# Performance work log

Measured on AMD Instinct MI355X. Metric: run time of the kernel, lower is better.

## Reference

```python
import jax, jax.numpy as jnp
import numpy as np

HEADS = 8
DIM_HEAD = 40
SCALE = DIM_HEAD ** -0.5


def setup_inputs() -> dict:
    key = jax.random.key(0)
    ks = jax.random.split(key, 6)
    B, S, D = 2, 4096, 320  # batch, seq (64x64 latent), query_dim
    inner = HEADS * DIM_HEAD  # 320
    s = 0.02
    return {
        "x": jax.random.normal(ks[0], (B, S, D), jnp.float32),
        "Wq": jax.random.normal(ks[1], (inner, D), jnp.float32) * s,
        "Wk": jax.random.normal(ks[2], (inner, D), jnp.float32) * s,
        "Wv": jax.random.normal(ks[3], (inner, D), jnp.float32) * s,
        "Wout": jax.random.normal(ks[4], (D, inner), jnp.float32) * s,
        "bout": jnp.zeros((D,), jnp.float32),
    }


def _split_heads(t):
    # [B, S, h*d] -> [B, h, S, d]
    B, S, _ = t.shape
    return t.reshape(B, S, HEADS, DIM_HEAD).transpose(0, 2, 1, 3)


def reference(x, Wq, Wk, Wv, Wout, bout):
    # self-attention path (context=None): k/v come from x
    q = _split_heads(x @ Wq.T)  # [B,h,S,d]
    k = _split_heads(x @ Wk.T)
    v = _split_heads(x @ Wv.T)
    # scores: materialized O(S^2) attention as in the torch einsum
    attn = jax.nn.softmax(jnp.einsum('bhid,bhjd->bhij', q, k) * SCALE, axis=-1)
    out = jnp.einsum('bhij,bhjd->bhid', attn, v)  # [B,h,S,d]
    B, _, S, _ = out.shape
    out = out.transpose(0, 2, 1, 3).reshape(B, S, HEADS * DIM_HEAD)
    return out @ Wout.T + bout  # to_out (dropout=0 -> identity)
```

## Files before the change

### kernel.cpp

```cpp
#include <hip/hip_runtime.h>

#define HEADS 8
#define DHEAD 40
#define SEQ   4096
#define BATCH 2
#define INNER 320
#define NBH   16
#define QSCALE ((float)(0.15811388300841897 * 1.4426950408889634))

typedef _Float16 f16;
typedef __attribute__((ext_vector_type(4)))  _Float16 half4;
typedef __attribute__((ext_vector_type(8)))  _Float16 half8;
typedef __attribute__((ext_vector_type(16))) float    f32x16;

#define XN4   (BATCH * SEQ * INNER / 4)
#define WQKV4 (3 * INNER * INNER / 4)
#define WOUT4 (INNER * INNER / 4)
#define CONV_TOTAL (XN4 + WQKV4 + WOUT4)

__global__ __launch_bounds__(256)
void convert_kernel(const float* __restrict__ x,
                    const float* __restrict__ Wq,
                    const float* __restrict__ Wk,
                    const float* __restrict__ Wv,
                    const float* __restrict__ Wout,
                    f16* __restrict__ xh, f16* __restrict__ wh,
                    f16* __restrict__ wouth)
{
    int i = blockIdx.x * 256 + threadIdx.x;
    if (i >= CONV_TOTAL) return;
    float4 v;
    f16* dst;
    float sc = 1.0f;
    if (i < XN4) {
        v = ((const float4*)x)[i];
        dst = xh + 4 * (size_t)i;
    } else if (i < XN4 + WQKV4) {
        int j = i - XN4;
        if (j < 25600)      { v = ((const float4*)Wq)[j]; sc = QSCALE; }
        else if (j < 51200) { v = ((const float4*)Wk)[j - 25600]; }
        else                { v = ((const float4*)Wv)[j - 51200]; }
        dst = wh + 4 * (size_t)j;
    } else {
        int j = i - XN4 - WQKV4;
        v = ((const float4*)Wout)[j];
        dst = wouth + 4 * (size_t)j;
    }
    half4 hh;
    hh.x = (f16)(v.x * sc); hh.y = (f16)(v.y * sc);
    hh.z = (f16)(v.z * sc); hh.w = (f16)(v.w * sc);
    *(half4*)dst = hh;
}

#define ASTR 72

__global__ __launch_bounds__(256)
void qkv_gemm_kernel(const f16* __restrict__ xh, const f16* __restrict__ wh,
                     f16* __restrict__ q, f16* __restrict__ k,
                     f16* __restrict__ vt)
{
    __shared__ f16 lds[(128 + 64) * ASTR];
    f16* As = lds;
    f16* Bs = lds + 128 * ASTR;

    const int tid  = threadIdx.x;
    const int m0   = blockIdx.y * 128;
    const int by   = blockIdx.x;
    const int wsel = by / 5;
    const int nb0  = (by % 5) * 64;
    const int wave = tid >> 6, lane = tid & 63, m = lane & 31, half = lane >> 5;

    f32x16 acc[2];
    #pragma unroll
    for (int i = 0; i < 16; i++) { acc[0][i] = 0.f; acc[1][i] = 0.f; }

    const f16* wbase = wh + (size_t)by * 64 * 320;

    for (int k0 = 0; k0 < 320; k0 += 64) {
        __syncthreads();
        #pragma unroll
        for (int u = 0; u < 4; u++) {
            int idx = tid + 256 * u;
            int r = idx >> 3, c8 = idx & 7;
            *(uint4*)&As[r * ASTR + c8 * 8] =
                *(const uint4*)&xh[(size_t)(m0 + r) * 320 + k0 + c8 * 8];
        }
        #pragma unroll
        for (int u = 0; u < 2; u++) {
            int idx = tid + 256 * u;
            int r = idx >> 3, c8 = idx & 7;
            *(uint4*)&Bs[r * ASTR + c8 * 8] =
                *(const uint4*)&wbase[(size_t)r * 320 + k0 + c8 * 8];
        }
        __syncthreads();
        #pragma unroll
        for (int c = 0; c < 4; c++) {
            half8 a  = *(const half8*)&As[(wave * 32 + m) * ASTR + c * 16 + half * 8];
            half8 b0 = *(const half8*)&Bs[m * ASTR + c * 16 + half * 8];
            half8 b1 = *(const half8*)&Bs[(32 + m) * ASTR + c * 16 + half * 8];
            acc[0] = __builtin_amdgcn_mfma_f32_32x32x16_f16(a, b0, acc[0], 0, 0, 0);
            acc[1] = __builtin_amdgcn_mfma_f32_32x32x16_f16(a, b1, acc[1], 0, 0, 0);
        }
    }

    if (wsel < 2) {
        f16* dst = (wsel == 0) ? q : k;
        #pragma unroll
        for (int nt = 0; nt < 2; nt++) {
            int nb = nb0 + nt * 32 + m;
            int h  = (nb * 205) >> 13;
            int dd = nb - h * 40;
            #pragma unroll
            for (int reg = 0; reg < 16; reg++) {
                int crow = 4 * half + (reg & 3) + 8 * (reg >> 2);
                int mg = m0 + wave * 32 + crow;
                int b = mg >> 12, s = mg & 4095;
                dst[((size_t)(b * 8 + h) * SEQ + s) * DHEAD + dd] = (f16)acc[nt][reg];
            }
        }
    } else {
        __syncthreads();
        f16* Ct = lds;
        #pragma unroll
        for (int nt = 0; nt < 2; nt++) {
            #pragma unroll
            for (int g = 0; g < 4; g++) {
                half4 hh;
                hh.x = (f16)acc[nt][4 * g + 0]; hh.y = (f16)acc[nt][4 * g + 1];
                hh.z = (f16)acc[nt][4 * g + 2]; hh.w = (f16)acc[nt][4 * g + 3];
                *(half4*)&Ct[(nt * 32 + m) * 136 + wave * 32 + 8 * g + 4 * half] = hh;
            }
        }
        __syncthreads();
        const int b = m0 >> 12, s0 = m0 & 4095;
        #pragma unroll
        for (int u = 0; u < 8; u++) {
            int idx = tid + 256 * u;
            int rl = idx >> 5, c4 = idx & 31;
            int nb = nb0 + rl;
            int h  = (nb * 205) >> 13;
            int dd = nb - h * 40;
            int w4 = c4 & 3;
            int c4p = (c4 & ~3) | ((w4 == 1) ? 2 : (w4 == 2) ? 1 : w4);
            *(uint2*)&vt[((size_t)(b * 8 + h) * DHEAD + dd) * SEQ + s0 + c4p * 4] =
                *(const uint2*)&Ct[rl * 136 + c4 * 4];
        }
    }
}

#define KSTR 56
#define VSTR 72
#define LDS_K 0
#define LDS_V 3584

__global__ __launch_bounds__(256, 4)
void attn_kernel(const f16* __restrict__ q, const f16* __restrict__ k,
                 const f16* __restrict__ vt, f16* __restrict__ y)
{
    __shared__ __align__(16) unsigned char ldsbuf[16896];
    f16*   ldsh = (f16*)ldsbuf;
    float* ldsf = (float*)ldsbuf;

    const int tid = threadIdx.x;
    const int blk = blockIdx.x;
    const int bh = blk >> 6, qt = blk & 63;
    const int b = bh >> 3, h = bh & 7;
    const int q0 = qt * 64;
    const int wave = tid >> 6, lane = tid & 63, m = lane & 31, half = lane >> 5;
    const int qs = wave >> 1, kh = wave & 1;

    if (tid < 128) {
        int key = tid >> 1, off = (tid & 1) * 4;
        *(uint2*)&ldsh[LDS_K + key * KSTR + 40 + off] = make_uint2(0u, 0u);
    }
    for (int i = tid; i < 24 * 16; i += 256) {
        int r = i >> 4, c = (i & 15) * 4;
        uint2 val = (r == 0) ? make_uint2(0x3C003C00u, 0x3C003C00u)
                             : make_uint2(0u, 0u);
        *(uint2*)&ldsh[LDS_V + (40 + r) * VSTR + c] = val;
    }

    half8 zero8;
    #pragma unroll
    for (int j = 0; j < 8; j++) zero8[j] = (f16)0.0f;
    half8 qa[3];
    {
        const f16* qb = q + ((size_t)bh * SEQ + q0 + qs * 32 + m) * DHEAD;
        qa[0] = *(const half8*)&qb[half * 8];
        qa[1] = *(const half8*)&qb[16 + half * 8];
        qa[2] = (half == 1) ? zero8 : *(const half8*)&qb[32];
    }

    f32x16 O[2];
    #pragma unroll
    for (int i = 0; i < 16; i++) { O[0][i] = 0.f; O[1][i] = 0.f; }

    const f16* kb = k  + (size_t)bh * SEQ * DHEAD;
    const f16* vb = vt + (size_t)bh * DHEAD * SEQ;

    const int krow0 = tid / 5,        kblk0 = tid % 5;
    const int krow1 = (256 + tid) / 5, kblk1 = (256 + tid) % 5;

    for (int j0 = 0; j0 < SEQ; j0 += 64) {
        __syncthreads();
        {
            uint4 t0 = *(const uint4*)&kb[(size_t)j0 * 40 + tid * 8];
            *(uint4*)&ldsh[LDS_K + krow0 * KSTR + kblk0 * 8] = t0;
            if (tid < 64) {
                uint4 t1 = *(const uint4*)&kb[(size_t)j0 * 40 + (256 + tid) * 8];
                *(uint4*)&ldsh[LDS_K + krow1 * KSTR + kblk1 * 8] = t1;
            }
        }
        {
            uint4 t0 = *(const uint4*)&vb[(size_t)(tid >> 3) * SEQ + j0 + (tid & 7) * 8];
            *(uint4*)&ldsh[LDS_V + (tid >> 3) * VSTR + (tid & 7) * 8] = t0;
            if (tid < 64) {
                int idx = 256 + tid;
                uint4 t1 = *(const uint4*)&vb[(size_t)(idx >> 3) * SEQ + j0 + (idx & 7) * 8];
                *(uint4*)&ldsh[LDS_V + (idx >> 3) * VSTR + (idx & 7) * 8] = t1;
            }
        }
        __syncthreads();

        f32x16 S;
        #pragma unroll
        for (int i = 0; i < 16; i++) S[i] = 0.f;
        #pragma unroll
        for (int c = 0; c < 3; c++) {
            half8 kf = *(const half8*)&ldsh[LDS_K + (kh * 32 + m) * KSTR + c * 16 + half * 8];
            S = __builtin_amdgcn_mfma_f32_32x32x16_f16(kf, qa[c], S, 0, 0, 0);
        }

        half8 p0, p1;
        #pragma unroll
        for (int j = 0; j < 8; j++) {
            p0[j] = (f16)exp2f(S[j]);
            p1[j] = (f16)exp2f(S[8 + j]);
        }

        #pragma unroll
        for (int c = 0; c < 2; c++) {
            half8 pc = c ? p1 : p0;
            half8 v0 = *(const half8*)&ldsh[LDS_V + m * VSTR + kh * 32 + c * 16 + half * 8];
            half8 v1 = *(const half8*)&ldsh[LDS_V + (32 + m) * VSTR + kh * 32 + c * 16 + half * 8];
            O[0] = __builtin_amdgcn_mfma_f32_32x32x16_f16(pc, v0, O[0], 0, 0, 0);
            O[1] = __builtin_amdgcn_mfma_f32_32x32x16_f16(pc, v1, O[1], 0, 0, 0);
        }
    }

    __syncthreads();
    if (kh == 1) {
        #pragma unroll
        for (int t = 0; t < 2; t++)
            #pragma unroll
            for (int reg = 0; reg < 16; reg++) {
                int row = 4 * half + (reg & 3) + 8 * (reg >> 2);
                ldsf[(qs * 32 + row) * 66 + t * 32 + m] = O[t][reg];
            }
    }
    __syncthreads();
    if (kh == 0) {
        #pragma unroll
        for (int t = 0; t < 2; t++)
            #pragma unroll
            for (int reg = 0; reg < 16; reg++) {
                int row = 4 * half + (reg & 3) + 8 * (reg >> 2);
                O[t][reg] += ldsf[(qs * 32 + row) * 66 + t * 32 + m];
            }
        #pragma unroll
        for (int reg = 0; reg < 16; reg++) {
            float l = __shfl(O[1][reg], 8 + 32 * half, 64);
            float rinv = 1.0f / l;
            int row = 4 * half + (reg & 3) + 8 * (reg >> 2);
            f16* yr = y + ((size_t)b * SEQ + q0 + qs * 32 + row) * INNER + h * DHEAD;
            yr[m] = (f16)(O[0][reg] * rinv);
            if (m < 8) yr[32 + m] = (f16)(O[1][reg] * rinv);
        }
    }
}

__global__ __launch_bounds__(256)
void out_proj_kernel(const f16* __restrict__ y, const f16* __restrict__ wouth,
                     const float* __restrict__ bout, float* __restrict__ out)
{
    __shared__ f16 lds[(128 + 64) * ASTR];
    f16* As = lds;
    f16* Bs = lds + 128 * ASTR;

    const int tid = threadIdx.x;
    const int m0 = blockIdx.y * 128;
    const int n0 = blockIdx.x * 64;
    const int wave = tid >> 6, lane = tid & 63, m = lane & 31, half = lane >> 5;

    f32x16 acc[2];
    #pragma unroll
    for (int i = 0; i < 16; i++) { acc[0][i] = 0.f; acc[1][i] = 0.f; }

    const f16* wbase = wouth + (size_t)n0 * 320;

    for (int k0 = 0; k0 < 320; k0 += 64) {
        __syncthreads();
        #pragma unroll
        for (int u = 0; u < 4; u++) {
            int idx = tid + 256 * u;
            int r = idx >> 3, c8 = idx & 7;
            *(uint4*)&As[r * ASTR + c8 * 8] =
                *(const uint4*)&y[(size_t)(m0 + r) * 320 + k0 + c8 * 8];
        }
        #pragma unroll
        for (int u = 0; u < 2; u++) {
            int idx = tid + 256 * u;
            int r = idx >> 3, c8 = idx & 7;
            *(uint4*)&Bs[r * ASTR + c8 * 8] =
                *(const uint4*)&wbase[(size_t)r * 320 + k0 + c8 * 8];
        }
        __syncthreads();
        #pragma unroll
        for (int c = 0; c < 4; c++) {
            half8 a  = *(const half8*)&As[(wave * 32 + m) * ASTR + c * 16 + half * 8];
            half8 b0 = *(const half8*)&Bs[m * ASTR + c * 16 + half * 8];
            half8 b1 = *(const half8*)&Bs[(32 + m) * ASTR + c * 16 + half * 8];
            acc[0] = __builtin_amdgcn_mfma_f32_32x32x16_f16(a, b0, acc[0], 0, 0, 0);
            acc[1] = __builtin_amdgcn_mfma_f32_32x32x16_f16(a, b1, acc[1], 0, 0, 0);
        }
    }

    #pragma unroll
    for (int nt = 0; nt < 2; nt++) {
        int n = n0 + nt * 32 + m;
        float bias = bout[n];
        #pragma unroll
        for (int reg = 0; reg < 16; reg++) {
            int crow = 4 * half + (reg & 3) + 8 * (reg >> 2);
            out[(size_t)(m0 + wave * 32 + crow) * 320 + n] = acc[nt][reg] + bias;
        }
    }
}

extern "C" void kernel_launch(void* const* d_in, const int* in_sizes, int n_in,
                              void* d_out, int out_size, void* d_ws, size_t ws_size,
                              hipStream_t stream)
{
    const float* x    = (const float*)d_in[0];
    const float* Wq   = (const float*)d_in[1];
    const float* Wk   = (const float*)d_in[2];
    const float* Wv   = (const float*)d_in[3];
    const float* Wout = (const float*)d_in[4];
    const float* bout = (const float*)d_in[5];
    float* out = (float*)d_out;

    unsigned char* ws = (unsigned char*)d_ws;
    f16* xh    = (f16*)(ws);
    f16* wh    = (f16*)(ws + 5242880);
    f16* wouth = (f16*)(ws + 5857280);
    f16* qd    = (f16*)(ws + 6062080);
    f16* kd    = (f16*)(ws + 11304960);
    f16* vtd   = (f16*)(ws + 16547840);
    f16* yd    = (f16*)(ws + 21790720);

    convert_kernel <<<2960,         256, 0, stream>>>(x, Wq, Wk, Wv, Wout, xh, wh, wouth);
    qkv_gemm_kernel<<<dim3(15, 64), 256, 0, stream>>>(xh, wh, qd, kd, vtd);
    attn_kernel    <<<1024,         256, 0, stream>>>(qd, kd, vtd, yd);
    out_proj_kernel<<<dim3(5, 64),  256, 0, stream>>>(yd, wouth, bout, out);
}
```

Before: 187.4 us.

## Fuse fp32-to-fp16 conversion into GEMM loads and prefetch K/V tiles in attention

Removes the standalone conversion kernel: the QKV and output-projection GEMMs now read fp32 x and weights directly and pack them to fp16 while staging into LDS, with the softmax scale applied to Wq on load. The attention loop gains a register prefetch of the next K/V tile so global loads overlap the MFMA and exp work. It also switches the exponential to the hardware exp2 builtin with packed round-toward-zero fp16 conversion. This saves a kernel launch and a pass through the fp16 copies, but doubles the GEMM input bytes read per tile, and x is re-read and re-converted by all 15 column blocks.

```diff
diff --git a/kernel.cpp b/kernel.cpp
--- a/kernel.cpp
+++ b/kernel.cpp
@@ -9,53 +9,36 @@
 #define QSCALE ((float)(0.15811388300841897 * 1.4426950408889634))
 
 typedef _Float16 f16;
+typedef __attribute__((ext_vector_type(2)))  __fp16   fp16x2;
 typedef __attribute__((ext_vector_type(4)))  _Float16 half4;
 typedef __attribute__((ext_vector_type(8)))  _Float16 half8;
 typedef __attribute__((ext_vector_type(16))) float    f32x16;
 
-#define XN4   (BATCH * SEQ * INNER / 4)
-#define WQKV4 (3 * INNER * INNER / 4)
-#define WOUT4 (INNER * INNER / 4)
-#define CONV_TOTAL (XN4 + WQKV4 + WOUT4)
+#if __has_builtin(__builtin_amdgcn_exp2f)
+#define EXP2F(x) __builtin_amdgcn_exp2f(x)
+#else
+#define EXP2F(x) exp2f(x)
+#endif
+
+union H8 { half8 h8; fp16x2 p2[4]; uint4 u4; };
+
+__device__ __forceinline__ uint4 pack8(float a0, float a1, float a2, float a3,
+                                       float a4, float a5, float a6, float a7) {
+    H8 u;
+    u.p2[0] = __builtin_amdgcn_cvt_pkrtz(a0, a1);
+    u.p2[1] = __builtin_amdgcn_cvt_pkrtz(a2, a3);
+    u.p2[2] = __builtin_amdgcn_cvt_pkrtz(a4, a5);
+    u.p2[3] = __builtin_amdgcn_cvt_pkrtz(a6, a7);
+    return u.u4;
+}
+
+#define ASTR 72
 
 __global__ __launch_bounds__(256)
-void convert_kernel(const float* __restrict__ x,
-                    const float* __restrict__ Wq,
-                    const float* __restrict__ Wk,
-                    const float* __restrict__ Wv,
-                    const float* __restrict__ Wout,
-                    f16* __restrict__ xh, f16* __restrict__ wh,
-                    f16* __restrict__ wouth)
-{
-    int i = blockIdx.x * 256 + threadIdx.x;
-    if (i >= CONV_TOTAL) return;
-    float4 v;
-    f16* dst;
-    float sc = 1.0f;
-    if (i < XN4) {
-        v = ((const float4*)x)[i];
-        dst = xh + 4 * (size_t)i;
-    } else if (i < XN4 + WQKV4) {
-        int j = i - XN4;
-        if (j < 25600)      { v = ((const float4*)Wq)[j]; sc = QSCALE; }
-        else if (j < 51200) { v = ((const float4*)Wk)[j - 25600]; }
-        else                { v = ((const float4*)Wv)[j - 51200]; }
-        dst = wh + 4 * (size_t)j;
-    } else {
-        int j = i - XN4 - WQKV4;
-        v = ((const float4*)Wout)[j];
-        dst = wouth + 4 * (size_t)j;
-    }
-    half4 hh;
-    hh.x = (f16)(v.x * sc); hh.y = (f16)(v.y * sc);
-    hh.z = (f16)(v.z * sc); hh.w = (f16)(v.w * sc);
-    *(half4*)dst = hh;
-}
-
-#define ASTR 72
-
-__global__ __launch_bounds__(256)
-void qkv_gemm_kernel(const f16* __restrict__ xh, const f16* __restrict__ wh,
+void qkv_gemm_kernel(const float* __restrict__ x,
+                     const float* __restrict__ Wq,
+                     const float* __restrict__ Wk,
+                     const float* __restrict__ Wv,
                      f16* __restrict__ q, f16* __restrict__ k,
                      f16* __restrict__ vt)
 {
@@ -70,27 +53,35 @@
     const int nb0  = (by % 5) * 64;
     const int wave = tid >> 6, lane = tid & 63, m = lane & 31, half = lane >> 5;
 
+    const float* __restrict__ W = (wsel == 0) ? Wq : (wsel == 1 ? Wk : Wv);
+    const float sc = (wsel == 0) ? QSCALE : 1.0f;
+
     f32x16 acc[2];
     #pragma unroll
     for (int i = 0; i < 16; i++) { acc[0][i] = 0.f; acc[1][i] = 0.f; }
 
-    const f16* wbase = wh + (size_t)by * 64 * 320;
-
     for (int k0 = 0; k0 < 320; k0 += 64) {
         __syncthreads();
         #pragma unroll
         for (int u = 0; u < 4; u++) {
             int idx = tid + 256 * u;
             int r = idx >> 3, c8 = idx & 7;
+            const float* src = &x[(size_t)(m0 + r) * 320 + k0 + c8 * 8];
+            float4 f0 = *(const float4*)src;
+            float4 f1 = *(const float4*)(src + 4);
             *(uint4*)&As[r * ASTR + c8 * 8] =
-                *(const uint4*)&xh[(size_t)(m0 + r) * 320 + k0 + c8 * 8];
+                pack8(f0.x, f0.y, f0.z, f0.w, f1.x, f1.y, f1.z, f1.w);
         }
         #pragma unroll
         for (int u = 0; u < 2; u++) {
             int idx = tid + 256 * u;
             int r = idx >> 3, c8 = idx & 7;
+            const float* src = &W[(size_t)(nb0 + r) * 320 + k0 + c8 * 8];
+            float4 f0 = *(const float4*)src;
+            float4 f1 = *(const float4*)(src + 4);
             *(uint4*)&Bs[r * ASTR + c8 * 8] =
-                *(const uint4*)&wbase[(size_t)r * 320 + k0 + c8 * 8];
+                pack8(f0.x * sc, f0.y * sc, f0.z * sc, f0.w * sc,
+                      f1.x * sc, f1.y * sc, f1.z * sc, f1.w * sc);
         }
         __syncthreads();
         #pragma unroll
@@ -198,29 +189,39 @@
     const f16* kb = k  + (size_t)bh * SEQ * DHEAD;
     const f16* vb = vt + (size_t)bh * DHEAD * SEQ;
 
-    const int krow0 = tid / 5,        kblk0 = tid % 5;
-    const int krow1 = (256 + tid) / 5, kblk1 = (256 + tid) % 5;
+    const int krow0 = tid / 5,          kblk0 = tid % 5;
+    const int krow1 = (256 + tid) / 5,  kblk1 = (256 + tid) % 5;
+    const int vrow0 = tid >> 3,         vblk0 = tid & 7;
+    const int vrow1 = (256 + tid) >> 3, vblk1 = (256 + tid) & 7;
+    const bool lo64 = (tid < 64);
+
+    uint4 ka0, ka1, va0, va1;
+    ka0 = *(const uint4*)&kb[(size_t)krow0 * DHEAD + kblk0 * 8];
+    va0 = *(const uint4*)&vb[(size_t)vrow0 * SEQ + vblk0 * 8];
+    if (lo64) {
+        ka1 = *(const uint4*)&kb[(size_t)krow1 * DHEAD + kblk1 * 8];
+        va1 = *(const uint4*)&vb[(size_t)vrow1 * SEQ + vblk1 * 8];
+    }
 
     for (int j0 = 0; j0 < SEQ; j0 += 64) {
         __syncthreads();
-        {
-            uint4 t0 = *(const uint4*)&kb[(size_t)j0 * 40 + tid * 8];
-            *(uint4*)&ldsh[LDS_K + krow0 * KSTR + kblk0 * 8] = t0;
-            if (tid < 64) {
-                uint4 t1 = *(const uint4*)&kb[(size_t)j0 * 40 + (256 + tid) * 8];
-                *(uint4*)&ldsh[LDS_K + krow1 * KSTR + kblk1 * 8] = t1;
-            }
-        }
-        {
-            uint4 t0 = *(const uint4*)&vb[(size_t)(tid >> 3) * SEQ + j0 + (tid & 7) * 8];
-            *(uint4*)&ldsh[LDS_V + (tid >> 3) * VSTR + (tid & 7) * 8] = t0;
-            if (tid < 64) {
-                int idx = 256 + tid;
-                uint4 t1 = *(const uint4*)&vb[(size_t)(idx >> 3) * SEQ + j0 + (idx & 7) * 8];
-                *(uint4*)&ldsh[LDS_V + (idx >> 3) * VSTR + (idx & 7) * 8] = t1;
-            }
-        }
-        __syncthreads();
+        *(uint4*)&ldsh[LDS_K + krow0 * KSTR + kblk0 * 8] = ka0;
+        *(uint4*)&ldsh[LDS_V + vrow0 * VSTR + vblk0 * 8] = va0;
+        if (lo64) {
+            *(uint4*)&ldsh[LDS_K + krow1 * KSTR + kblk1 * 8] = ka1;
+            *(uint4*)&ldsh[LDS_V + vrow1 * VSTR + vblk1 * 8] = va1;
+        }
+        __syncthreads();
+
+        if (j0 + 64 < SEQ) {
+            const int jn = j0 + 64;
+            ka0 = *(const uint4*)&kb[(size_t)(jn + krow0) * DHEAD + kblk0 * 8];
+            va0 = *(const uint4*)&vb[(size_t)vrow0 * SEQ + jn + vblk0 * 8];
+            if (lo64) {
+                ka1 = *(const uint4*)&kb[(size_t)(jn + krow1) * DHEAD + kblk1 * 8];
+                va1 = *(const uint4*)&vb[(size_t)vrow1 * SEQ + jn + vblk1 * 8];
+            }
+        }
 
         f32x16 S;
         #pragma unroll
@@ -231,16 +232,16 @@
             S = __builtin_amdgcn_mfma_f32_32x32x16_f16(kf, qa[c], S, 0, 0, 0);
         }
 
-        half8 p0, p1;
-        #pragma unroll
-        for (int j = 0; j < 8; j++) {
-            p0[j] = (f16)exp2f(S[j]);
-            p1[j] = (f16)exp2f(S[8 + j]);
+        H8 p0u, p1u;
+        #pragma unroll
+        for (int g = 0; g < 4; g++) {
+            p0u.p2[g] = __builtin_amdgcn_cvt_pkrtz(EXP2F(S[2 * g]),     EXP2F(S[2 * g + 1]));
+            p1u.p2[g] = __builtin_amdgcn_cvt_pkrtz(EXP2F(S[8 + 2 * g]), EXP2F(S[9 + 2 * g]));
         }
 
         #pragma unroll
         for (int c = 0; c < 2; c++) {
-            half8 pc = c ? p1 : p0;
+            half8 pc = c ? p1u.h8 : p0u.h8;
             half8 v0 = *(const half8*)&ldsh[LDS_V + m * VSTR + kh * 32 + c * 16 + half * 8];
             half8 v1 = *(const half8*)&ldsh[LDS_V + (32 + m) * VSTR + kh * 32 + c * 16 + half * 8];
             O[0] = __builtin_amdgcn_mfma_f32_32x32x16_f16(pc, v0, O[0], 0, 0, 0);
@@ -280,7 +281,7 @@
 }
 
 __global__ __launch_bounds__(256)
-void out_proj_kernel(const f16* __restrict__ y, const f16* __restrict__ wouth,
+void out_proj_kernel(const f16* __restrict__ y, const float* __restrict__ Wout,
                      const float* __restrict__ bout, float* __restrict__ out)
 {
     __shared__ f16 lds[(128 + 64) * ASTR];
@@ -296,8 +297,6 @@
     #pragma unroll
     for (int i = 0; i < 16; i++) { acc[0][i] = 0.f; acc[1][i] = 0.f; }
 
-    const f16* wbase = wouth + (size_t)n0 * 320;
-
     for (int k0 = 0; k0 < 320; k0 += 64) {
         __syncthreads();
         #pragma unroll
@@ -311,8 +310,11 @@
         for (int u = 0; u < 2; u++) {
             int idx = tid + 256 * u;
             int r = idx >> 3, c8 = idx & 7;
+            const float* src = &Wout[(size_t)(n0 + r) * 320 + k0 + c8 * 8];
+            float4 f0 = *(const float4*)src;
+            float4 f1 = *(const float4*)(src + 4);
             *(uint4*)&Bs[r * ASTR + c8 * 8] =
-                *(const uint4*)&wbase[(size_t)r * 320 + k0 + c8 * 8];
+                pack8(f0.x, f0.y, f0.z, f0.w, f1.x, f1.y, f1.z, f1.w);
         }
         __syncthreads();
         #pragma unroll
@@ -350,16 +352,12 @@
     float* out = (float*)d_out;
 
     unsigned char* ws = (unsigned char*)d_ws;
-    f16* xh    = (f16*)(ws);
-    f16* wh    = (f16*)(ws + 5242880);
-    f16* wouth = (f16*)(ws + 5857280);
-    f16* qd    = (f16*)(ws + 6062080);
-    f16* kd    = (f16*)(ws + 11304960);
-    f16* vtd   = (f16*)(ws + 16547840);
-    f16* yd    = (f16*)(ws + 21790720);
-
-    convert_kernel <<<2960,         256, 0, stream>>>(x, Wq, Wk, Wv, Wout, xh, wh, wouth);
-    qkv_gemm_kernel<<<dim3(15, 64), 256, 0, stream>>>(xh, wh, qd, kd, vtd);
+    f16* qd  = (f16*)(ws);
+    f16* kd  = (f16*)(ws + 5242880);
+    f16* vtd = (f16*)(ws + 10485760);
+    f16* yd  = (f16*)(ws + 15728640);
+
+    qkv_gemm_kernel<<<dim3(15, 64), 256, 0, stream>>>(x, Wq, Wk, Wv, qd, kd, vtd);
     attn_kernel    <<<1024,         256, 0, stream>>>(qd, kd, vtd, yd);
-    out_proj_kernel<<<dim3(5, 64),  256, 0, stream>>>(yd, wouth, bout, out);
-}
+    out_proj_kernel<<<dim3(5, 64),  256, 0, stream>>>(yd, Wout, bout, out);
+}
```

After: 172.9 us. 1.08x faster.
